# Optimization experiments

Measured on AMD Instinct MI355X. Metric: run time of the kernel, lower is better.

The kernel has to match this reference:

```python
import jax, jax.numpy as jnp
import numpy as np

LAMBDA_MAX = 2.0  # standard re-scaled Laplacian assumption (DGL lambda_max=[2])
NUM_GRAPHS = 100


def _cheb(feat, src, dst, d_invsqrt, W, b):
    # DGL ChebConv: h = sum_i fc_i(X_i) + b, X_i = Chebyshev recursion on scaled Laplacian
    n = feat.shape[0]
    k = W.shape[0]
    re = 2.0 / LAMBDA_MAX

    def aggr(f):  # D^{-1/2} A D^{-1/2} f  via gather + segment_sum
        fh = f * d_invsqrt
        m = jax.ops.segment_sum(fh[src], dst, num_segments=n)
        return m * d_invsqrt

    X0 = feat
    h = X0 @ W[0]
    if k > 1:
        X1 = -re * aggr(X0) + X0 * (re - 1.0)
        h = h + X1 @ W[1]
        for i in range(2, k):
            Xi = -2.0 * re * aggr(X1) + X1 * (2.0 * (re - 1.0)) - X0
            h = h + Xi @ W[i]
            X0, X1 = X1, Xi
    return h + b


def _edgeconv(feat, src, dst, Wt, bt, Wp, bp):
    # DGL EdgeConv: out_i = max_{j->i} [theta(x_i - x_j) + phi(x_i)], 0 if no in-edges
    n = feat.shape[0]
    theta = (feat[dst] - feat[src]) @ Wt + bt           # [E, H]
    phi = feat @ Wp + bp                                # [N, H]
    msg = theta + phi[dst]                              # [E, H]
    agg = jax.ops.segment_max(msg, dst, num_segments=n)
    return jnp.where(jnp.isfinite(agg), agg, jnp.zeros((), feat.dtype))


def setup_inputs() -> dict:
    key = jax.random.key(0)
    ks = jax.random.split(key, 20)
    N, E, G = 100000, 1600000, NUM_GRAPHS
    IN, H, K = 16, 64, 3

    def lin(k, fan_in, shape):
        return jax.random.normal(k, shape, dtype=jnp.float32) * (1.0 / np.sqrt(fan_in))

    inp = {}
    inp["feat"] = jax.random.normal(ks[0], (N, IN), dtype=jnp.float32)
    inp["src"] = jax.random.randint(ks[1], (E,), 0, N)
    inp["dst"] = jax.random.randint(ks[2], (E,), 0, N)
    inp["graph_ids"] = jnp.sort(jax.random.randint(ks[3], (N,), 0, G))
    # ChebConv params: W [k, in, out], b [out]
    inp["W1"] = lin(ks[4], IN, (K, IN, H)); inp["b1"] = jnp.zeros((H,), jnp.float32)
    inp["W2"] = lin(ks[5], H, (K, H, H));   inp["b2"] = jnp.zeros((H,), jnp.float32)
    inp["W3"] = lin(ks[6], H, (K, H, H));   inp["b3"] = jnp.zeros((H,), jnp.float32)
    # EdgeConv params: theta + phi linears
    inp["Wt1"] = lin(ks[7], H, (H, H));  inp["bt1"] = jnp.zeros((H,), jnp.float32)
    inp["Wp1"] = lin(ks[8], H, (H, H));  inp["bp1"] = jnp.zeros((H,), jnp.float32)
    inp["Wt2"] = lin(ks[9], H, (H, H));  inp["bt2"] = jnp.zeros((H,), jnp.float32)
    inp["Wp2"] = lin(ks[10], H, (H, H)); inp["bp2"] = jnp.zeros((H,), jnp.float32)
    return inp


def reference(feat, src, dst, graph_ids, W1, b1, W2, b2, W3, b3,
              Wt1, bt1, Wp1, bp1, Wt2, bt2, Wp2, bp2):
    n = feat.shape[0]
    deg = jax.ops.segment_sum(jnp.ones((src.shape[0],), feat.dtype), dst, num_segments=n)
    d_invsqrt = (jnp.clip(deg, 1.0, None) ** -0.5)[:, None]  # [N, 1]

    h = jax.nn.relu(_cheb(feat, src, dst, d_invsqrt, W1, b1))
    h = jax.nn.relu(_edgeconv(h, src, dst, Wt1, bt1, Wp1, bp1))
    h = jax.nn.relu(_cheb(h, src, dst, d_invsqrt, W2, b2))
    h = jax.nn.relu(_edgeconv(h, src, dst, Wt2, bt2, Wp2, bp2))
    h = jax.nn.relu(_cheb(h, src, dst, d_invsqrt, W3, b3))

    # dgl.mean_nodes: per-graph mean pooling
    counts = jax.ops.segment_sum(jnp.ones((n,), h.dtype), graph_ids, num_segments=NUM_GRAPHS)
    hg = jax.ops.segment_sum(h, graph_ids, num_segments=NUM_GRAPHS)
    return hg / jnp.clip(counts, 1.0, None)[:, None]
```

## Files before the change

kernel.cpp:

```cpp
#include <hip/hip_runtime.h>
#include <hip/hip_bf16.h>
#include <math.h>

typedef __attribute__((ext_vector_type(8))) short short8;
typedef __attribute__((ext_vector_type(4))) float floatx4;

__device__ __forceinline__ unsigned short bfb(float x) {
    union { __hip_bfloat16 h; unsigned short u; } c;
    c.h = __float2bfloat16(x);
    return c.u;
}
__device__ __forceinline__ float bf2f(unsigned short u) {
    union { unsigned int i; float f; } c;
    c.i = ((unsigned int)u) << 16;
    return c.f;
}
__device__ __forceinline__ void acc2(float& lo, float& hi, unsigned d) {
    union { unsigned u; float f; } a, b;
    a.u = d << 16;
    b.u = d & 0xffff0000u;
    lo += a.f; hi += b.f;
}
__device__ __forceinline__ unsigned pkmaxu16(unsigned a, unsigned b) {
    unsigned d;
    asm("v_pk_max_u16 %0, %1, %2" : "=v"(d) : "v"(a), "v"(b));
    return d;
}


__global__ __launch_bounds__(256) void k_bhist(const int* __restrict__ dst, int* __restrict__ bcnt, int E) {
    __shared__ int h[512];
    int t = threadIdx.x;
    for (int i = t; i < 512; i += 256) h[i] = 0;
    __syncthreads();
    int step = gridDim.x * 256;
    for (int i = blockIdx.x * 256 + t; i < E; i += step) atomicAdd(&h[dst[i] >> 8], 1);
    __syncthreads();
    for (int i = t; i < 512; i += 256) if (h[i]) atomicAdd(&bcnt[i], h[i]);
}

__global__ __launch_bounds__(512) void k_scanBkt(const int* __restrict__ bcnt, int* __restrict__ boff,
                                                 int* __restrict__ bcur, int nb, int E) {
    __shared__ int s[512];
    int t = threadIdx.x;
    int v = (t < nb) ? bcnt[t] : 0;
    s[t] = v;
    __syncthreads();
    for (int off = 1; off < 512; off <<= 1) {
        int x = (t >= off) ? s[t - off] : 0;
        __syncthreads();
        s[t] += x;
        __syncthreads();
    }
    if (t < nb) { boff[t] = s[t] - v; bcur[t] = s[t] - v; }
    if (t == 0) boff[nb] = E;
}

#define PCHUNK 8192

__global__ __launch_bounds__(256) void k_partA(const int* __restrict__ src, const int* __restrict__ dst,
                                               int* __restrict__ bcur, unsigned* __restrict__ ebuf, int E) {
    __shared__ int h[512];
    __shared__ int base[512];
    int t = threadIdx.x;
    for (int i = t; i < 512; i += 256) h[i] = 0;
    __syncthreads();
    int start = blockIdx.x * PCHUNK;
    int end = start + PCHUNK < E ? start + PCHUNK : E;
    for (int i = start + t; i < end; i += 256) atomicAdd(&h[dst[i] >> 8], 1);
    __syncthreads();
    for (int i = t; i < 512; i += 256) {
        int c = h[i];
        base[i] = c ? atomicAdd(&bcur[i], c) : 0;
        h[i] = 0;
    }
    __syncthreads();
    for (int i = start + t; i < end; i += 256) {
        int d = dst[i];
        int b = d >> 8;
        int r = atomicAdd(&h[b], 1);
        ebuf[base[b] + r] = ((unsigned)src[i] << 8) | (unsigned)(d & 255);
    }
}

__global__ __launch_bounds__(256) void k_finish(const unsigned* __restrict__ ebuf, const int* __restrict__ boff,
                                                int* __restrict__ row_off, float* __restrict__ dinv,
                                                float* __restrict__ dsq, int* __restrict__ csr,
                                                const float* __restrict__ feat, unsigned short* __restrict__ hd,
                                                int N, int E) {
    __shared__ int h[256];
    __shared__ int sc[256];
    __shared__ int cur[256];
    int b = blockIdx.x, t = threadIdx.x;
    h[t] = 0;
    __syncthreads();
    int beg = boff[b], end = boff[b + 1];
    for (int e = beg + t; e < end; e += 256) atomicAdd(&h[ebuf[e] & 255], 1);
    __syncthreads();
    int v = h[t];
    sc[t] = v;
    __syncthreads();
    for (int off = 1; off < 256; off <<= 1) {
        int x = (t >= off) ? sc[t - off] : 0;
        __syncthreads();
        sc[t] += x;
        __syncthreads();
    }
    int node = (b << 8) + t;
    int excl = beg + sc[t] - v;
    if (node < N) {
        row_off[node] = excl;
        float dg = (float)(v > 1 ? v : 1);
        float dv = rsqrtf(dg);
        dinv[node] = dv;
        dsq[node] = sqrtf(dg);
        const float* f = &feat[(size_t)node * 16];
#pragma unroll
        for (int k = 0; k < 16; k += 4) {
            float4 x = *(const float4*)&f[k];
            ushort4 u = { bfb(x.x * dv), bfb(x.y * dv), bfb(x.z * dv), bfb(x.w * dv) };
            *(ushort4*)&hd[(size_t)node * 16 + k] = u;
        }
    }
    cur[t] = excl;
    if (b == 0 && t == 0) row_off[N] = E;
    __syncthreads();
    for (int e = beg + t; e < end; e += 256) {
        unsigned ed = ebuf[e];
        int pos = atomicAdd(&cur[ed & 255], 1);
        csr[pos] = (int)(ed >> 8);
    }
}


__global__ __launch_bounds__(256) void k_aggr16(const unsigned short* __restrict__ Xd, const float* __restrict__ Z,
                                                const float* __restrict__ dinv,
                                                const int* __restrict__ row_off, const int* __restrict__ csr,
                                                unsigned short* __restrict__ outb, unsigned short* __restrict__ outd,
                                                float alpha, float beta, int zoff, int N) {
    int node = blockIdx.x * 4 + (threadIdx.x >> 6);
    if (node >= N) return;
    int lane = threadIdx.x & 63;
    int g = lane >> 2;
    int co = (lane & 3) * 8;
    int beg = row_off[node], end = row_off[node + 1];
    int deg = end - beg;
    int myOff = (lane < deg) ? (csr[beg + lane] << 5) : zoff;
    const char* base = (const char*)Xd + co;
    float a0 = 0.f, a1 = 0.f, a2 = 0.f, a3 = 0.f;
    {
        int o0 = __shfl(myOff, g);
        int o1 = __shfl(myOff, 16 + g);
        ushort4 x0 = *(const ushort4*)(base + o0);
        ushort4 x1 = *(const ushort4*)(base + o1);
        a0 += bf2f(x0.x); a1 += bf2f(x0.y); a2 += bf2f(x0.z); a3 += bf2f(x0.w);
        a0 += bf2f(x1.x); a1 += bf2f(x1.y); a2 += bf2f(x1.z); a3 += bf2f(x1.w);
    }
    if (deg > 32) {
        int dmain = deg < 64 ? deg : 64;
        for (int j = 32; j < dmain; j += 16) {
            int o = __shfl(myOff, j + g);
            ushort4 x = *(const ushort4*)(base + o);
            a0 += bf2f(x.x); a1 += bf2f(x.y); a2 += bf2f(x.z); a3 += bf2f(x.w);
        }
        for (int e = beg + 64; e < end; e += 16) {
            int idx = e + g;
            int s = csr[idx < end ? idx : end - 1];
            ushort4 x = *(const ushort4*)(base + (s << 5));
            if (idx < end) {
                a0 += bf2f(x.x); a1 += bf2f(x.y); a2 += bf2f(x.z); a3 += bf2f(x.w);
            }
        }
    }
    a0 += __shfl_xor(a0, 4); a0 += __shfl_xor(a0, 8); a0 += __shfl_xor(a0, 16); a0 += __shfl_xor(a0, 32);
    a1 += __shfl_xor(a1, 4); a1 += __shfl_xor(a1, 8); a1 += __shfl_xor(a1, 16); a1 += __shfl_xor(a1, 32);
    a2 += __shfl_xor(a2, 4); a2 += __shfl_xor(a2, 8); a2 += __shfl_xor(a2, 16); a2 += __shfl_xor(a2, 32);
    a3 += __shfl_xor(a3, 4); a3 += __shfl_xor(a3, 8); a3 += __shfl_xor(a3, 16); a3 += __shfl_xor(a3, 32);
    if (g == 0) {
        int c4 = (lane & 3) * 4;
        float dn = dinv[node];
        float v0 = alpha * dn * a0;
        float v1 = alpha * dn * a1;
        float v2 = alpha * dn * a2;
        float v3 = alpha * dn * a3;
        if (Z) {
            float4 zv = *(const float4*)&Z[(size_t)node * 16 + c4];
            v0 += beta * zv.x; v1 += beta * zv.y; v2 += beta * zv.z; v3 += beta * zv.w;
        }
        ushort4 ub = { bfb(v0), bfb(v1), bfb(v2), bfb(v3) };
        *(ushort4*)&outb[(size_t)node * 16 + c4] = ub;
        if (outd) {
            ushort4 u = { bfb(v0 * dn), bfb(v1 * dn), bfb(v2 * dn), bfb(v3 * dn) };
            *(ushort4*)&outd[(size_t)node * 16 + c4] = u;
        }
    }
}


__global__ __launch_bounds__(256) void k_aggr64(const unsigned short* __restrict__ Xd,
                                                const unsigned short* __restrict__ Z,
                                                const float* __restrict__ dinv,
                                                const int* __restrict__ row_off, const int* __restrict__ csr,
                                                unsigned short* __restrict__ outb, unsigned short* __restrict__ outd,
                                                float alpha, float beta, int zoff, int N) {
    int node = blockIdx.x * 4 + (threadIdx.x >> 6);
    if (node >= N) return;
    int lane = threadIdx.x & 63;
    int g = lane >> 3;
    int co = (lane & 7) * 16;
    int beg = row_off[node], end = row_off[node + 1];
    int deg = end - beg;
    int myOff = (lane < deg) ? (csr[beg + lane] << 7) : zoff;
    const char* base = (const char*)Xd + co;
    float a0 = 0.f, a1 = 0.f, a2 = 0.f, a3 = 0.f, a4 = 0.f, a5 = 0.f, a6 = 0.f, a7 = 0.f;
    {
        int o0 = __shfl(myOff, g);
        int o1 = __shfl(myOff, 8 + g);
        int o2 = __shfl(myOff, 16 + g);
        int o3 = __shfl(myOff, 24 + g);
        uint4 x0 = *(const uint4*)(base + o0);
        uint4 x1 = *(const uint4*)(base + o1);
        uint4 x2 = *(const uint4*)(base + o2);
        uint4 x3 = *(const uint4*)(base + o3);
        acc2(a0, a1, x0.x); acc2(a2, a3, x0.y); acc2(a4, a5, x0.z); acc2(a6, a7, x0.w);
        acc2(a0, a1, x1.x); acc2(a2, a3, x1.y); acc2(a4, a5, x1.z); acc2(a6, a7, x1.w);
        acc2(a0, a1, x2.x); acc2(a2, a3, x2.y); acc2(a4, a5, x2.z); acc2(a6, a7, x2.w);
        acc2(a0, a1, x3.x); acc2(a2, a3, x3.y); acc2(a4, a5, x3.z); acc2(a6, a7, x3.w);
    }
    if (deg > 32) {
        int dmain = deg < 64 ? deg : 64;
        for (int j = 32; j < dmain; j += 8) {
            int o = __shfl(myOff, j + g);
            uint4 x = *(const uint4*)(base + o);
            acc2(a0, a1, x.x); acc2(a2, a3, x.y); acc2(a4, a5, x.z); acc2(a6, a7, x.w);
        }
        for (int e = beg + 64; e < end; e += 8) {
            int idx = e + g;
            int s = csr[idx < end ? idx : end - 1];
            uint4 x = *(const uint4*)(base + (s << 7));
            if (idx < end) {
                acc2(a0, a1, x.x); acc2(a2, a3, x.y); acc2(a4, a5, x.z); acc2(a6, a7, x.w);
            }
        }
    }
    a0 += __shfl_xor(a0, 8); a0 += __shfl_xor(a0, 16); a0 += __shfl_xor(a0, 32);
    a1 += __shfl_xor(a1, 8); a1 += __shfl_xor(a1, 16); a1 += __shfl_xor(a1, 32);
    a2 += __shfl_xor(a2, 8); a2 += __shfl_xor(a2, 16); a2 += __shfl_xor(a2, 32);
    a3 += __shfl_xor(a3, 8); a3 += __shfl_xor(a3, 16); a3 += __shfl_xor(a3, 32);
    a4 += __shfl_xor(a4, 8); a4 += __shfl_xor(a4, 16); a4 += __shfl_xor(a4, 32);
    a5 += __shfl_xor(a5, 8); a5 += __shfl_xor(a5, 16); a5 += __shfl_xor(a5, 32);
    a6 += __shfl_xor(a6, 8); a6 += __shfl_xor(a6, 16); a6 += __shfl_xor(a6, 32);
    a7 += __shfl_xor(a7, 8); a7 += __shfl_xor(a7, 16); a7 += __shfl_xor(a7, 32);
    if (g == 0) {
        float dn = dinv[node];
        float v[8] = { a0, a1, a2, a3, a4, a5, a6, a7 };
#pragma unroll
        for (int i = 0; i < 8; ++i) v[i] *= alpha * dn;
        size_t rb = (size_t)node * 128 + co;
        if (Z) {
            uint4 zv = *(const uint4*)((const char*)Z + rb);
            unsigned zd[4] = { zv.x, zv.y, zv.z, zv.w };
#pragma unroll
            for (int i = 0; i < 4; ++i) {
                union { unsigned u; float f; } lo, hi;
                lo.u = zd[i] << 16; hi.u = zd[i] & 0xffff0000u;
                v[2 * i] += beta * lo.f;
                v[2 * i + 1] += beta * hi.f;
            }
        }
        if (outb) {
            uint4 ub;
            unsigned* pb = (unsigned*)&ub;
#pragma unroll
            for (int i = 0; i < 4; ++i)
                pb[i] = (unsigned)bfb(v[2 * i]) | ((unsigned)bfb(v[2 * i + 1]) << 16);
            *(uint4*)((char*)outb + rb) = ub;
        }
        if (outd) {
            uint4 ud;
            unsigned* pd = (unsigned*)&ud;
#pragma unroll
            for (int i = 0; i < 4; ++i)
                pd[i] = (unsigned)bfb(v[2 * i] * dn) | ((unsigned)bfb(v[2 * i + 1] * dn) << 16);
            *(uint4*)((char*)outd + rb) = ud;
        }
    }
}


template <int KDIM, bool FUSE_E1, bool POOLOUT>
__global__ __launch_bounds__(256) void k_cheb(const void* __restrict__ X0v, const void* __restrict__ X1v,
                                              const void* __restrict__ X2v, const float* __restrict__ dsq,
                                              const float* __restrict__ W, const float* __restrict__ bvec,
                                              const float* __restrict__ Wt, const float* __restrict__ Wp,
                                              const float* __restrict__ bt, const float* __restrict__ bp,
                                              unsigned short* __restrict__ md, unsigned short* __restrict__ pbuf,
                                              const int* __restrict__ gid, float* __restrict__ out, int N) {
    constexpr int KT = (KDIM == 16) ? 64 : 3 * KDIM;
    constexpr int SX = KT + 8;
    constexpr int PH1 = 2 * 64 * SX;
    constexpr int PH2 = FUSE_E1 ? (64 * 72 + 128 * 72) : 0;
    constexpr int SSZ = PH1 > PH2 ? PH1 : PH2;
    constexpr bool hasMid = (KDIM == 64);
    __shared__ unsigned short S[SSZ];
    unsigned short* Xs = S;
    unsigned short* Ws = S + 64 * SX;
    int t = threadIdx.x;

    {
        int sn = t & 63;
        int gn = blockIdx.x * 64 + sn; if (gn >= N) gn = N - 1;
        int k0 = (t >> 6) * (KDIM / 4);
        if constexpr (KDIM == 16) {
            float4 v = *(const float4*)&((const float*)X0v)[(size_t)gn * 16 + k0];
            ushort4 u = { bfb(v.x), bfb(v.y), bfb(v.z), bfb(v.w) };
            *(ushort4*)&Xs[sn * SX + k0] = u;
            *(ushort4*)&Xs[sn * SX + 16 + k0] =
                *(const ushort4*)&((const unsigned short*)X1v)[(size_t)gn * 16 + k0];
            *(ushort4*)&Xs[sn * SX + 32 + k0] =
                *(const ushort4*)&((const unsigned short*)X2v)[(size_t)gn * 16 + k0];
            int kp = 48 + (t >> 6) * 4;
            ushort4 z = { 0, 0, 0, 0 };
            *(ushort4*)&Xs[sn * SX + kp] = z;
        } else {
            const unsigned short* Xp[3] = { (const unsigned short*)X0v, (const unsigned short*)X1v,
                                            (const unsigned short*)X2v };
#pragma unroll
            for (int a = 0; a < 3; ++a) {
#pragma unroll
                for (int i = 0; i < KDIM / 16; ++i) {
                    *(ushort4*)&Xs[sn * SX + a * KDIM + k0 + 4 * i] =
                        *(const ushort4*)&Xp[a][(size_t)gn * KDIM + k0 + 4 * i];
                }
            }
        }
    }
    for (int idx = t; idx < 3 * KDIM * 64; idx += 256) {
        int a = idx / (KDIM * 64);
        int r = idx % (KDIM * 64);
        int k = r >> 6, n = r & 63;
        Ws[n * SX + a * KDIM + k] = bfb(W[idx]);
    }
    if constexpr (KDIM == 16) {
        for (int idx = t; idx < 1024; idx += 256) {
            int n = idx & 63, k = 48 + (idx >> 6);
            Ws[n * SX + k] = 0;
        }
    }
    __syncthreads();

    int wave = t >> 6, lane = t & 63;
    int fi = lane & 15, quad = lane >> 4;
    int arow = wave * 16 + fi;

    floatx4 accA[4], accM[4];
#pragma unroll
    for (int i = 0; i < 4; ++i) { accA[i] = (floatx4){0.f,0.f,0.f,0.f}; accM[i] = (floatx4){0.f,0.f,0.f,0.f}; }
#pragma unroll
    for (int ks = 0; ks < KT / 32; ++ks) {
        short8 af = *(const short8*)&Xs[arow * SX + ks * 32 + quad * 8];
        short8 b0 = *(const short8*)&Ws[(0 * 16 + fi) * SX + ks * 32 + quad * 8];
        short8 b1 = *(const short8*)&Ws[(1 * 16 + fi) * SX + ks * 32 + quad * 8];
        short8 b2 = *(const short8*)&Ws[(2 * 16 + fi) * SX + ks * 32 + quad * 8];
        short8 b3 = *(const short8*)&Ws[(3 * 16 + fi) * SX + ks * 32 + quad * 8];
        if (hasMid && ks >= 2 && ks < 4) {
            accM[0] = __builtin_amdgcn_mfma_f32_16x16x32_bf16(af, b0, accM[0], 0, 0, 0);
            accM[1] = __builtin_amdgcn_mfma_f32_16x16x32_bf16(af, b1, accM[1], 0, 0, 0);
            accM[2] = __builtin_amdgcn_mfma_f32_16x16x32_bf16(af, b2, accM[2], 0, 0, 0);
            accM[3] = __builtin_amdgcn_mfma_f32_16x16x32_bf16(af, b3, accM[3], 0, 0, 0);
        } else {
            accA[0] = __builtin_amdgcn_mfma_f32_16x16x32_bf16(af, b0, accA[0], 0, 0, 0);
            accA[1] = __builtin_amdgcn_mfma_f32_16x16x32_bf16(af, b1, accA[1], 0, 0, 0);
            accA[2] = __builtin_amdgcn_mfma_f32_16x16x32_bf16(af, b2, accA[2], 0, 0, 0);
            accA[3] = __builtin_amdgcn_mfma_f32_16x16x32_bf16(af, b3, accA[3], 0, 0, 0);
        }
    }

    int nbase0 = blockIdx.x * 64 + wave * 16;
    int nbase = nbase0 + quad * 4;
    float dd[4];
#pragma unroll
    for (int reg = 0; reg < 4; ++reg) {
        if constexpr (hasMid) {
            int node = nbase + reg;
            dd[reg] = dsq[node < N ? node : N - 1];
        } else dd[reg] = 0.f;
    }
    float rv[4][4];
#pragma unroll
    for (int nt = 0; nt < 4; ++nt) {
        int col = nt * 16 + fi;
        float bias = bvec[col];
#pragma unroll
        for (int reg = 0; reg < 4; ++reg) {
            float v = accA[nt][reg] + bias;
            if constexpr (hasMid) v += accM[nt][reg] * dd[reg];
            rv[nt][reg] = fmaxf(v, 0.f);
        }
    }

    if constexpr (POOLOUT) {
        int gfirst = gid[nbase0 < N ? nbase0 : N - 1];
        int lastn = nbase0 + 15;
        int glast = gid[lastn < N ? lastn : N - 1];
        bool uniform = (lastn < N) && (gfirst == glast);
        if (uniform) {
#pragma unroll
            for (int nt = 0; nt < 4; ++nt) {
                float s = (rv[nt][0] + rv[nt][1]) + (rv[nt][2] + rv[nt][3]);
                s += __shfl_xor(s, 16); s += __shfl_xor(s, 32);
                if (quad == 0) atomicAdd(&out[(size_t)gfirst * 64 + nt * 16 + fi], s);
            }
        } else {
#pragma unroll
            for (int reg = 0; reg < 4; ++reg) {
                int node = nbase + reg;
                if (node < N) {
                    int g = gid[node];
#pragma unroll
                    for (int nt = 0; nt < 4; ++nt)
                        atomicAdd(&out[(size_t)g * 64 + nt * 16 + fi], rv[nt][reg]);
                }
            }
        }
    } else if constexpr (FUSE_E1) {
        __syncthreads();
        unsigned short* Hs = S;
        unsigned short* W2l = S + 64 * 72;
        int lrow = wave * 16 + quad * 4;
#pragma unroll
        for (int nt = 0; nt < 4; ++nt)
#pragma unroll
            for (int reg = 0; reg < 4; ++reg)
                Hs[(lrow + reg) * 72 + nt * 16 + fi] = bfb(rv[nt][reg]);
        for (int idx = t; idx < 4096; idx += 256) {
            int k = idx >> 6, n = idx & 63;
            float wt = Wt[idx];
            W2l[n * 72 + k] = bfb(wt);
            W2l[(64 + n) * 72 + k] = bfb(wt + Wp[idx]);
        }
        __syncthreads();
        floatx4 ae[8];
#pragma unroll
        for (int i = 0; i < 8; ++i) ae[i] = (floatx4){0.f,0.f,0.f,0.f};
#pragma unroll
        for (int ks = 0; ks < 2; ++ks) {
            short8 af = *(const short8*)&Hs[arow * 72 + ks * 32 + quad * 8];
#pragma unroll
            for (int nt = 0; nt < 8; ++nt) {
                short8 bf = *(const short8*)&W2l[(nt * 16 + fi) * 72 + ks * 32 + quad * 8];
                ae[nt] = __builtin_amdgcn_mfma_f32_16x16x32_bf16(af, bf, ae[nt], 0, 0, 0);
            }
        }
#pragma unroll
        for (int nt = 0; nt < 8; ++nt) {
            int col = nt * 16 + fi;
            if (col < 64) {
#pragma unroll
                for (int reg = 0; reg < 4; ++reg) {
                    int node = nbase + reg;
                    if (node < N) {
                        unsigned u = (unsigned)bfb(ae[nt][reg]) ^ 0x8000u;
                        unsigned key = (u & 0x8000u) ? (~u & 0xffffu) : (u | 0x8000u);
                        md[(size_t)node * 64 + col] = (unsigned short)key;
                    }
                }
            } else {
                int cc = col - 64;
                float bias2 = bt[cc] + bp[cc];
#pragma unroll
                for (int reg = 0; reg < 4; ++reg) {
                    int node = nbase + reg;
                    if (node < N) pbuf[(size_t)node * 64 + cc] = bfb(ae[nt][reg] + bias2);
                }
            }
        }
    }
}


__global__ __launch_bounds__(256) void k_e2_b(const unsigned short* __restrict__ md,
                                              const unsigned short* __restrict__ pbuf,
                                              const int* __restrict__ row_off, const int* __restrict__ csr,
                                              const float* __restrict__ dinv, unsigned short* __restrict__ out,
                                              unsigned short* __restrict__ outd, int zoff, int N) {
    int node = blockIdx.x * 4 + (threadIdx.x >> 6);
    if (node >= N) return;
    int lane = threadIdx.x & 63;
    int g = lane >> 3;
    int co = (lane & 7) * 16;
    int beg = row_off[node], end = row_off[node + 1];
    int deg = end - beg;
    int dmain = deg < 64 ? deg : 64;
    int li = lane < dmain ? lane : dmain - 1;
    int myOff = (deg > 0) ? (csr[beg + li] << 7) : zoff;
    const char* base = (const char*)md + co;
    unsigned k0 = 0, k1 = 0, k2 = 0, k3 = 0;
    {
        int o0 = __shfl(myOff, g);
        int o1 = __shfl(myOff, 8 + g);
        int o2 = __shfl(myOff, 16 + g);
        int o3 = __shfl(myOff, 24 + g);
        uint4 x0 = *(const uint4*)(base + o0);
        uint4 x1 = *(const uint4*)(base + o1);
        uint4 x2 = *(const uint4*)(base + o2);
        uint4 x3 = *(const uint4*)(base + o3);
        k0 = pkmaxu16(k0, x0.x); k1 = pkmaxu16(k1, x0.y); k2 = pkmaxu16(k2, x0.z); k3 = pkmaxu16(k3, x0.w);
        k0 = pkmaxu16(k0, x1.x); k1 = pkmaxu16(k1, x1.y); k2 = pkmaxu16(k2, x1.z); k3 = pkmaxu16(k3, x1.w);
        k0 = pkmaxu16(k0, x2.x); k1 = pkmaxu16(k1, x2.y); k2 = pkmaxu16(k2, x2.z); k3 = pkmaxu16(k3, x2.w);
        k0 = pkmaxu16(k0, x3.x); k1 = pkmaxu16(k1, x3.y); k2 = pkmaxu16(k2, x3.z); k3 = pkmaxu16(k3, x3.w);
    }
    if (deg > 32) {
        for (int j = 32; j < dmain; j += 8) {
            int o = __shfl(myOff, j + g);
            uint4 x = *(const uint4*)(base + o);
            k0 = pkmaxu16(k0, x.x); k1 = pkmaxu16(k1, x.y); k2 = pkmaxu16(k2, x.z); k3 = pkmaxu16(k3, x.w);
        }
        for (int e = beg + 64; e < end; e += 8) {
            int idx = e + g;
            int s = csr[idx < end ? idx : end - 1];
            uint4 x = *(const uint4*)(base + (s << 7));
            k0 = pkmaxu16(k0, x.x); k1 = pkmaxu16(k1, x.y); k2 = pkmaxu16(k2, x.z); k3 = pkmaxu16(k3, x.w);
        }
    }
    k0 = pkmaxu16(k0, __shfl_xor((int)k0, 8)); k0 = pkmaxu16(k0, __shfl_xor((int)k0, 16)); k0 = pkmaxu16(k0, __shfl_xor((int)k0, 32));
    k1 = pkmaxu16(k1, __shfl_xor((int)k1, 8)); k1 = pkmaxu16(k1, __shfl_xor((int)k1, 16)); k1 = pkmaxu16(k1, __shfl_xor((int)k1, 32));
    k2 = pkmaxu16(k2, __shfl_xor((int)k2, 8)); k2 = pkmaxu16(k2, __shfl_xor((int)k2, 16)); k2 = pkmaxu16(k2, __shfl_xor((int)k2, 32));
    k3 = pkmaxu16(k3, __shfl_xor((int)k3, 8)); k3 = pkmaxu16(k3, __shfl_xor((int)k3, 16)); k3 = pkmaxu16(k3, __shfl_xor((int)k3, 32));
    if (g == 0) {
        unsigned kd[4] = { k0, k1, k2, k3 };
        float a[8];
#pragma unroll
        for (int i = 0; i < 4; ++i) {
            unsigned klo = kd[i] & 0xffffu, khi = kd[i] >> 16;
            unsigned short tlo = (klo & 0x8000u) ? (unsigned short)(klo & 0x7fffu) : (unsigned short)(~klo & 0xffffu);
            unsigned short thi = (khi & 0x8000u) ? (unsigned short)(khi & 0x7fffu) : (unsigned short)(~khi & 0xffffu);
            a[2 * i] = bf2f(tlo);
            a[2 * i + 1] = bf2f(thi);
        }
        float r[8];
        if (end > beg) {
            uint4 pk = *(const uint4*)((const char*)pbuf + (size_t)node * 128 + co);
            unsigned pd4[4] = { pk.x, pk.y, pk.z, pk.w };
#pragma unroll
            for (int i = 0; i < 4; ++i) {
                r[2 * i]     = fmaxf(bf2f((unsigned short)(pd4[i] & 0xffffu)) + a[2 * i], 0.f);
                r[2 * i + 1] = fmaxf(bf2f((unsigned short)(pd4[i] >> 16)) + a[2 * i + 1], 0.f);
            }
        } else {
#pragma unroll
            for (int i = 0; i < 8; ++i) r[i] = 0.f;
        }
        float dn = dinv[node];
        size_t rb = (size_t)node * 128 + co;
        uint4 ub, ud;
        unsigned* pb = (unsigned*)&ub;
        unsigned* pd = (unsigned*)&ud;
#pragma unroll
        for (int i = 0; i < 4; ++i) {
            pb[i] = (unsigned)bfb(r[2 * i]) | ((unsigned)bfb(r[2 * i + 1]) << 16);
            pd[i] = (unsigned)bfb(r[2 * i] * dn) | ((unsigned)bfb(r[2 * i + 1] * dn) << 16);
        }
        *(uint4*)((char*)out + rb) = ub;
        *(uint4*)((char*)outd + rb) = ud;
    }
}


__global__ __launch_bounds__(256) void k_div(float* __restrict__ out, const int* __restrict__ gid,
                                             int N, int total) {
    int i = blockIdx.x * blockDim.x + threadIdx.x;
    if (i >= total) return;
    int g = i >> 6;
    int lo = 0, hi = N;
    while (lo < hi) { int m = (lo + hi) >> 1; if (gid[m] < g) lo = m + 1; else hi = m; }
    int s = lo;
    hi = N;
    while (lo < hi) { int m = (lo + hi) >> 1; if (gid[m] < g + 1) lo = m + 1; else hi = m; }
    float c = (float)(lo - s);
    out[i] /= fmaxf(c, 1.f);
}


extern "C" void kernel_launch(void* const* d_in, const int* in_sizes, int n_in,
                              void* d_out, int out_size, void* d_ws, size_t ws_size,
                              hipStream_t stream) {
    const float* feat = (const float*)d_in[0];
    const int* src = (const int*)d_in[1];
    const int* dst = (const int*)d_in[2];
    const int* gid = (const int*)d_in[3];
    const float* W1 = (const float*)d_in[4];  const float* b1 = (const float*)d_in[5];
    const float* W2 = (const float*)d_in[6];  const float* b2 = (const float*)d_in[7];
    const float* W3 = (const float*)d_in[8];  const float* b3 = (const float*)d_in[9];
    const float* Wt1 = (const float*)d_in[10]; const float* bt1 = (const float*)d_in[11];
    const float* Wp1 = (const float*)d_in[12]; const float* bp1 = (const float*)d_in[13];
    const float* Wt2 = (const float*)d_in[14]; const float* bt2 = (const float*)d_in[15];
    const float* Wp2 = (const float*)d_in[16]; const float* bp2 = (const float*)d_in[17];
    float* out = (float*)d_out;

    const int N = in_sizes[0] / 16;
    const int E = in_sizes[1];
    const int nb = (N + 255) >> 8;

    char* p = (char*)d_ws;
    auto alloc = [&](size_t nbytes) {
        void* r = (void*)p;
        p += (nbytes + 255) & ~(size_t)255;
        return r;
    };
    int* bcnt     = (int*)alloc(512 * 4);
    char* zpage   = (char*)alloc(256);
    size_t zspan  = (size_t)((char*)zpage - (char*)bcnt) + 256;
    int* boff     = (int*)alloc(513 * 4);
    int* bcur     = (int*)alloc(512 * 4);
    int* row_off  = (int*)alloc((size_t)(N + 1) * 4);
    int* csr      = (int*)alloc((size_t)E * 4);
    float* dinv   = (float*)alloc((size_t)N * 4);
    float* dsq    = (float*)alloc((size_t)N * 4);
    float* bufA   = (float*)alloc((size_t)N * 64 * 4);
    float* bufB   = (float*)alloc((size_t)N * 64 * 4);
    float* bufC   = (float*)alloc((size_t)N * 64 * 4);
    float* bufD   = (float*)alloc((size_t)N * 64 * 4);
    unsigned short* md   = (unsigned short*)alloc((size_t)N * 64 * 2);
    unsigned short* pbuf = (unsigned short*)alloc((size_t)N * 64 * 2);

    unsigned* ebuf = (unsigned*)bufA;
    unsigned short* hd = (unsigned short*)bufC;
    unsigned short* xd = hd + (size_t)N * 64;
    unsigned short* xA16 = (unsigned short*)bufA;
    unsigned short* xB16 = (unsigned short*)bufB;
    unsigned short* xd3 = (unsigned short*)bufA;
    unsigned short* hD = (unsigned short*)bufD;

    const int zo_hd = (int)((char*)zpage - (char*)hd);
    const int zo_xd = (int)((char*)zpage - (char*)xd);
    const int zo_xd3 = (int)((char*)zpage - (char*)xd3);
    const int zo_md = (int)((char*)zpage - (char*)md);

    hipMemsetAsync(bcnt, 0, zspan, stream);
    hipMemsetAsync(d_out, 0, (size_t)out_size * 4, stream);

    const int nbw = (N + 3) / 4;
    const int nbt = (N + 63) / 64;
    const int npart = (E + PCHUNK - 1) / PCHUNK;

    k_bhist<<<256, 256, 0, stream>>>(dst, bcnt, E);
    k_scanBkt<<<1, 512, 0, stream>>>(bcnt, boff, bcur, nb, E);
    k_partA<<<npart, 256, 0, stream>>>(src, dst, bcur, ebuf, E);
    k_finish<<<nb, 256, 0, stream>>>(ebuf, boff, row_off, dinv, dsq, csr, feat, hd, N, E);

    k_aggr16<<<nbw, 256, 0, stream>>>(hd, nullptr, dinv, row_off, csr, xA16, xd, -1.f, 0.f, zo_hd, N);
    k_aggr16<<<nbw, 256, 0, stream>>>(xd, feat, dinv, row_off, csr, xB16, nullptr, -2.f, -1.f, zo_xd, N);
    k_cheb<16, true, false><<<nbt, 256, 0, stream>>>(feat, xA16, xB16, nullptr, W1, b1,
                                                     Wt1, Wp1, bt1, bp1, md, pbuf, nullptr, nullptr, N);
    k_e2_b<<<nbw, 256, 0, stream>>>(md, pbuf, row_off, csr, dinv, hD, hd, zo_md, N);

    k_aggr64<<<nbw, 256, 0, stream>>>(hd, nullptr, dinv, row_off, csr, nullptr, xd, -1.f, 0.f, zo_hd, N);
    k_aggr64<<<nbw, 256, 0, stream>>>(xd, hD, dinv, row_off, csr, xB16, nullptr, -2.f, -1.f, zo_xd, N);
    k_cheb<64, true, false><<<nbt, 256, 0, stream>>>(hD, xd, xB16, dsq, W2, b2,
                                                     Wt2, Wp2, bt2, bp2, md, pbuf, nullptr, nullptr, N);
    k_e2_b<<<nbw, 256, 0, stream>>>(md, pbuf, row_off, csr, dinv, hD, hd, zo_md, N);

    k_aggr64<<<nbw, 256, 0, stream>>>(hd, nullptr, dinv, row_off, csr, nullptr, xd3, -1.f, 0.f, zo_hd, N);
    k_aggr64<<<nbw, 256, 0, stream>>>(xd3, hD, dinv, row_off, csr, xB16, nullptr, -2.f, -1.f, zo_xd3, N);
    k_cheb<64, false, true><<<nbt, 256, 0, stream>>>(hD, xd3, xB16, dsq, W3, b3,
                                                     nullptr, nullptr, nullptr, nullptr,
                                                     nullptr, nullptr, gid, out, N);

    k_div<<<(out_size + 255) / 256, 256, 0, stream>>>(out, gid, N, out_size);
}
```

Measured before the change: 533.7 us.

## Fuse second Chebyshev aggregation into cheb GEMM and drop CSR bucket prepass

The second neighbour aggregation of each Chebyshev layer now runs inside the GEMM kernel: each block gathers its 64 rows into shared memory before the MFMA, so the X2 intermediate is never written to or read back from global memory. The bucket histogram and scan kernels are removed by giving each 256-node bucket a fixed slab of SLABC slots, and row offsets become begin/end pairs. Pooling accumulates into a workspace buffer so the separate output memset can be dropped. The trade-offs are that gather latency now sits inside the GEMM blocks, which have lower parallelism than the standalone aggregation kernels, and the fixed slab size assumes no bucket ever receives more than 5120 edges.

```diff
diff --git a/kernel.cpp b/kernel.cpp
--- a/kernel.cpp
+++ b/kernel.cpp
@@ -27,36 +27,9 @@
     return d;
 }
 
-
-__global__ __launch_bounds__(256) void k_bhist(const int* __restrict__ dst, int* __restrict__ bcnt, int E) {
-    __shared__ int h[512];
-    int t = threadIdx.x;
-    for (int i = t; i < 512; i += 256) h[i] = 0;
-    __syncthreads();
-    int step = gridDim.x * 256;
-    for (int i = blockIdx.x * 256 + t; i < E; i += step) atomicAdd(&h[dst[i] >> 8], 1);
-    __syncthreads();
-    for (int i = t; i < 512; i += 256) if (h[i]) atomicAdd(&bcnt[i], h[i]);
-}
-
-__global__ __launch_bounds__(512) void k_scanBkt(const int* __restrict__ bcnt, int* __restrict__ boff,
-                                                 int* __restrict__ bcur, int nb, int E) {
-    __shared__ int s[512];
-    int t = threadIdx.x;
-    int v = (t < nb) ? bcnt[t] : 0;
-    s[t] = v;
-    __syncthreads();
-    for (int off = 1; off < 512; off <<= 1) {
-        int x = (t >= off) ? s[t - off] : 0;
-        __syncthreads();
-        s[t] += x;
-        __syncthreads();
-    }
-    if (t < nb) { boff[t] = s[t] - v; bcur[t] = s[t] - v; }
-    if (t == 0) boff[nb] = E;
-}
-
+#define SLABC 5120
 #define PCHUNK 8192
+
 
 __global__ __launch_bounds__(256) void k_partA(const int* __restrict__ src, const int* __restrict__ dst,
                                                int* __restrict__ bcur, unsigned* __restrict__ ebuf, int E) {
@@ -79,22 +52,22 @@
         int d = dst[i];
         int b = d >> 8;
         int r = atomicAdd(&h[b], 1);
-        ebuf[base[b] + r] = ((unsigned)src[i] << 8) | (unsigned)(d & 255);
-    }
-}
-
-__global__ __launch_bounds__(256) void k_finish(const unsigned* __restrict__ ebuf, const int* __restrict__ boff,
-                                                int* __restrict__ row_off, float* __restrict__ dinv,
+        ebuf[b * SLABC + base[b] + r] = ((unsigned)src[i] << 8) | (unsigned)(d & 255);
+    }
+}
+
+__global__ __launch_bounds__(256) void k_finish(const unsigned* __restrict__ ebuf, const int* __restrict__ bcur,
+                                                int2* __restrict__ row_be, float* __restrict__ dinv,
                                                 float* __restrict__ dsq, int* __restrict__ csr,
                                                 const float* __restrict__ feat, unsigned short* __restrict__ hd,
-                                                int N, int E) {
+                                                int N) {
     __shared__ int h[256];
     __shared__ int sc[256];
     __shared__ int cur[256];
     int b = blockIdx.x, t = threadIdx.x;
     h[t] = 0;
     __syncthreads();
-    int beg = boff[b], end = boff[b + 1];
+    int beg = b * SLABC, end = beg + bcur[b];
     for (int e = beg + t; e < end; e += 256) atomicAdd(&h[ebuf[e] & 255], 1);
     __syncthreads();
     int v = h[t];
@@ -109,7 +82,7 @@
     int node = (b << 8) + t;
     int excl = beg + sc[t] - v;
     if (node < N) {
-        row_off[node] = excl;
+        row_be[node] = make_int2(excl, excl + v);
         float dg = (float)(v > 1 ? v : 1);
         float dv = rsqrtf(dg);
         dinv[node] = dv;
@@ -123,7 +96,6 @@
         }
     }
     cur[t] = excl;
-    if (b == 0 && t == 0) row_off[N] = E;
     __syncthreads();
     for (int e = beg + t; e < end; e += 256) {
         unsigned ed = ebuf[e];
@@ -133,17 +105,18 @@
 }
 
 
-__global__ __launch_bounds__(256) void k_aggr16(const unsigned short* __restrict__ Xd, const float* __restrict__ Z,
+__global__ __launch_bounds__(256) void k_aggr16(const unsigned short* __restrict__ Xd,
                                                 const float* __restrict__ dinv,
-                                                const int* __restrict__ row_off, const int* __restrict__ csr,
+                                                const int2* __restrict__ row_be, const int* __restrict__ csr,
                                                 unsigned short* __restrict__ outb, unsigned short* __restrict__ outd,
-                                                float alpha, float beta, int zoff, int N) {
+                                                int zoff, int N) {
     int node = blockIdx.x * 4 + (threadIdx.x >> 6);
     if (node >= N) return;
     int lane = threadIdx.x & 63;
     int g = lane >> 2;
     int co = (lane & 3) * 8;
-    int beg = row_off[node], end = row_off[node + 1];
+    int2 be = row_be[node];
+    int beg = be.x, end = be.y;
     int deg = end - beg;
     int myOff = (lane < deg) ? (csr[beg + lane] << 5) : zoff;
     const char* base = (const char*)Xd + co;
@@ -179,36 +152,26 @@
     if (g == 0) {
         int c4 = (lane & 3) * 4;
         float dn = dinv[node];
-        float v0 = alpha * dn * a0;
-        float v1 = alpha * dn * a1;
-        float v2 = alpha * dn * a2;
-        float v3 = alpha * dn * a3;
-        if (Z) {
-            float4 zv = *(const float4*)&Z[(size_t)node * 16 + c4];
-            v0 += beta * zv.x; v1 += beta * zv.y; v2 += beta * zv.z; v3 += beta * zv.w;
-        }
+        float v0 = -dn * a0, v1 = -dn * a1, v2 = -dn * a2, v3 = -dn * a3;
         ushort4 ub = { bfb(v0), bfb(v1), bfb(v2), bfb(v3) };
         *(ushort4*)&outb[(size_t)node * 16 + c4] = ub;
-        if (outd) {
-            ushort4 u = { bfb(v0 * dn), bfb(v1 * dn), bfb(v2 * dn), bfb(v3 * dn) };
-            *(ushort4*)&outd[(size_t)node * 16 + c4] = u;
-        }
+        ushort4 u = { bfb(v0 * dn), bfb(v1 * dn), bfb(v2 * dn), bfb(v3 * dn) };
+        *(ushort4*)&outd[(size_t)node * 16 + c4] = u;
     }
 }
 
 
 __global__ __launch_bounds__(256) void k_aggr64(const unsigned short* __restrict__ Xd,
-                                                const unsigned short* __restrict__ Z,
                                                 const float* __restrict__ dinv,
-                                                const int* __restrict__ row_off, const int* __restrict__ csr,
-                                                unsigned short* __restrict__ outb, unsigned short* __restrict__ outd,
-                                                float alpha, float beta, int zoff, int N) {
+                                                const int2* __restrict__ row_be, const int* __restrict__ csr,
+                                                unsigned short* __restrict__ outd, int zoff, int N) {
     int node = blockIdx.x * 4 + (threadIdx.x >> 6);
     if (node >= N) return;
     int lane = threadIdx.x & 63;
     int g = lane >> 3;
     int co = (lane & 7) * 16;
-    int beg = row_off[node], end = row_off[node + 1];
+    int2 be = row_be[node];
+    int beg = be.x, end = be.y;
     int deg = end - beg;
     int myOff = (lane < deg) ? (csr[beg + lane] << 7) : zoff;
     const char* base = (const char*)Xd + co;
@@ -254,116 +217,324 @@
     if (g == 0) {
         float dn = dinv[node];
         float v[8] = { a0, a1, a2, a3, a4, a5, a6, a7 };
-#pragma unroll
-        for (int i = 0; i < 8; ++i) v[i] *= alpha * dn;
-        size_t rb = (size_t)node * 128 + co;
-        if (Z) {
-            uint4 zv = *(const uint4*)((const char*)Z + rb);
-            unsigned zd[4] = { zv.x, zv.y, zv.z, zv.w };
-#pragma unroll
-            for (int i = 0; i < 4; ++i) {
-                union { unsigned u; float f; } lo, hi;
-                lo.u = zd[i] << 16; hi.u = zd[i] & 0xffff0000u;
-                v[2 * i] += beta * lo.f;
-                v[2 * i + 1] += beta * hi.f;
-            }
-        }
-        if (outb) {
-            uint4 ub;
-            unsigned* pb = (unsigned*)&ub;
-#pragma unroll
-            for (int i = 0; i < 4; ++i)
-                pb[i] = (unsigned)bfb(v[2 * i]) | ((unsigned)bfb(v[2 * i + 1]) << 16);
-            *(uint4*)((char*)outb + rb) = ub;
-        }
-        if (outd) {
-            uint4 ud;
-            unsigned* pd = (unsigned*)&ud;
-#pragma unroll
-            for (int i = 0; i < 4; ++i)
-                pd[i] = (unsigned)bfb(v[2 * i] * dn) | ((unsigned)bfb(v[2 * i + 1] * dn) << 16);
-            *(uint4*)((char*)outd + rb) = ud;
-        }
-    }
-}
-
-
-template <int KDIM, bool FUSE_E1, bool POOLOUT>
-__global__ __launch_bounds__(256) void k_cheb(const void* __restrict__ X0v, const void* __restrict__ X1v,
-                                              const void* __restrict__ X2v, const float* __restrict__ dsq,
-                                              const float* __restrict__ W, const float* __restrict__ bvec,
-                                              const float* __restrict__ Wt, const float* __restrict__ Wp,
-                                              const float* __restrict__ bt, const float* __restrict__ bp,
-                                              unsigned short* __restrict__ md, unsigned short* __restrict__ pbuf,
-                                              const int* __restrict__ gid, float* __restrict__ out, int N) {
-    constexpr int KT = (KDIM == 16) ? 64 : 3 * KDIM;
-    constexpr int SX = KT + 8;
-    constexpr int PH1 = 2 * 64 * SX;
-    constexpr int PH2 = FUSE_E1 ? (64 * 72 + 128 * 72) : 0;
-    constexpr int SSZ = PH1 > PH2 ? PH1 : PH2;
-    constexpr bool hasMid = (KDIM == 64);
-    __shared__ unsigned short S[SSZ];
-    unsigned short* Xs = S;
-    unsigned short* Ws = S + 64 * SX;
+        uint4 ud;
+        unsigned* pd = (unsigned*)&ud;
+#pragma unroll
+        for (int i = 0; i < 4; ++i) {
+            float lo = -dn * dn * v[2 * i];
+            float hi = -dn * dn * v[2 * i + 1];
+            pd[i] = (unsigned)bfb(lo) | ((unsigned)bfb(hi) << 16);
+        }
+        *(uint4*)((char*)outd + (size_t)node * 128 + co) = ud;
+    }
+}
+
+
+__global__ __launch_bounds__(256) void k_cheb16f(const float* __restrict__ feat,
+                                                 const unsigned short* __restrict__ X1b,
+                                                 const unsigned short* __restrict__ xd,
+                                                 const int2* __restrict__ row_be, const int* __restrict__ csr,
+                                                 const float* __restrict__ dinv,
+                                                 const float* __restrict__ W, const float* __restrict__ bvec,
+                                                 const float* __restrict__ Wt, const float* __restrict__ Wp,
+                                                 const float* __restrict__ bt, const float* __restrict__ bp,
+                                                 unsigned short* __restrict__ md, unsigned short* __restrict__ pbuf,
+                                                 int zoff, int N) {
+    constexpr int SX = 72;
+    __shared__ unsigned short S[13824];
+    unsigned short* Ws = S;
+    unsigned short* Xs2 = S + 64 * 72;
     int t = threadIdx.x;
+    int wave = t >> 6, lane = t & 63;
+
+    for (int idx = t; idx < 3072; idx += 256) {
+        int a = idx >> 10;
+        int r = idx & 1023;
+        int k = r >> 6, n = r & 63;
+        Ws[n * SX + a * 16 + k] = bfb(W[idx]);
+    }
+    for (int idx = t; idx < 1024; idx += 256) {
+        int n = idx & 63, k = 48 + (idx >> 6);
+        Ws[n * SX + k] = 0;
+    }
 
     {
-        int sn = t & 63;
-        int gn = blockIdx.x * 64 + sn; if (gn >= N) gn = N - 1;
-        int k0 = (t >> 6) * (KDIM / 4);
-        if constexpr (KDIM == 16) {
-            float4 v = *(const float4*)&((const float*)X0v)[(size_t)gn * 16 + k0];
-            ushort4 u = { bfb(v.x), bfb(v.y), bfb(v.z), bfb(v.w) };
-            *(ushort4*)&Xs[sn * SX + k0] = u;
-            *(ushort4*)&Xs[sn * SX + 16 + k0] =
-                *(const ushort4*)&((const unsigned short*)X1v)[(size_t)gn * 16 + k0];
-            *(ushort4*)&Xs[sn * SX + 32 + k0] =
-                *(const ushort4*)&((const unsigned short*)X2v)[(size_t)gn * 16 + k0];
-            int kp = 48 + (t >> 6) * 4;
-            ushort4 z = { 0, 0, 0, 0 };
-            *(ushort4*)&Xs[sn * SX + kp] = z;
-        } else {
-            const unsigned short* Xp[3] = { (const unsigned short*)X0v, (const unsigned short*)X1v,
-                                            (const unsigned short*)X2v };
-#pragma unroll
-            for (int a = 0; a < 3; ++a) {
-#pragma unroll
-                for (int i = 0; i < KDIM / 16; ++i) {
-                    *(ushort4*)&Xs[sn * SX + a * KDIM + k0 + 4 * i] =
-                        *(const ushort4*)&Xp[a][(size_t)gn * KDIM + k0 + 4 * i];
+        int g = lane >> 2;
+        int co = (lane & 3) * 8;
+        const char* base = (const char*)xd + co;
+        for (int i = 0; i < 16; ++i) {
+            int ln = wave * 16 + i;
+            int gn = blockIdx.x * 64 + ln; if (gn >= N) gn = N - 1;
+            int2 be = row_be[gn];
+            int beg = be.x, end = be.y;
+            int deg = end - beg;
+            int myOff = (lane < deg) ? (csr[beg + lane] << 5) : zoff;
+            float a0 = 0.f, a1 = 0.f, a2 = 0.f, a3 = 0.f;
+            {
+                int o0 = __shfl(myOff, g);
+                int o1 = __shfl(myOff, 16 + g);
+                ushort4 x0 = *(const ushort4*)(base + o0);
+                ushort4 x1 = *(const ushort4*)(base + o1);
+                a0 += bf2f(x0.x); a1 += bf2f(x0.y); a2 += bf2f(x0.z); a3 += bf2f(x0.w);
+                a0 += bf2f(x1.x); a1 += bf2f(x1.y); a2 += bf2f(x1.z); a3 += bf2f(x1.w);
+            }
+            if (deg > 32) {
+                int dmain = deg < 64 ? deg : 64;
+                for (int j = 32; j < dmain; j += 16) {
+                    int o = __shfl(myOff, j + g);
+                    ushort4 x = *(const ushort4*)(base + o);
+                    a0 += bf2f(x.x); a1 += bf2f(x.y); a2 += bf2f(x.z); a3 += bf2f(x.w);
                 }
-            }
-        }
-    }
-    for (int idx = t; idx < 3 * KDIM * 64; idx += 256) {
-        int a = idx / (KDIM * 64);
-        int r = idx % (KDIM * 64);
-        int k = r >> 6, n = r & 63;
-        Ws[n * SX + a * KDIM + k] = bfb(W[idx]);
-    }
-    if constexpr (KDIM == 16) {
-        for (int idx = t; idx < 1024; idx += 256) {
-            int n = idx & 63, k = 48 + (idx >> 6);
-            Ws[n * SX + k] = 0;
-        }
-    }
-    __syncthreads();
-
-    int wave = t >> 6, lane = t & 63;
+                for (int e = beg + 64; e < end; e += 16) {
+                    int idx = e + g;
+                    int s = csr[idx < end ? idx : end - 1];
+                    ushort4 x = *(const ushort4*)(base + (s << 5));
+                    if (idx < end) {
+                        a0 += bf2f(x.x); a1 += bf2f(x.y); a2 += bf2f(x.z); a3 += bf2f(x.w);
+                    }
+                }
+            }
+            a0 += __shfl_xor(a0, 4); a0 += __shfl_xor(a0, 8); a0 += __shfl_xor(a0, 16); a0 += __shfl_xor(a0, 32);
+            a1 += __shfl_xor(a1, 4); a1 += __shfl_xor(a1, 8); a1 += __shfl_xor(a1, 16); a1 += __shfl_xor(a1, 32);
+            a2 += __shfl_xor(a2, 4); a2 += __shfl_xor(a2, 8); a2 += __shfl_xor(a2, 16); a2 += __shfl_xor(a2, 32);
+            a3 += __shfl_xor(a3, 4); a3 += __shfl_xor(a3, 8); a3 += __shfl_xor(a3, 16); a3 += __shfl_xor(a3, 32);
+            if (g == 0) {
+                int c4 = (lane & 3) * 4;
+                float dn = dinv[gn];
+                float4 zv = *(const float4*)&feat[(size_t)gn * 16 + c4];
+                float v0 = -2.f * dn * a0 - zv.x;
+                float v1 = -2.f * dn * a1 - zv.y;
+                float v2 = -2.f * dn * a2 - zv.z;
+                float v3 = -2.f * dn * a3 - zv.w;
+                ushort4 u = { bfb(v0), bfb(v1), bfb(v2), bfb(v3) };
+                *(ushort4*)&Xs2[ln * 24 + c4] = u;
+            }
+        }
+    }
+    __syncthreads();
+
     int fi = lane & 15, quad = lane >> 4;
     int arow = wave * 16 + fi;
+    int arow_node = blockIdx.x * 64 + arow;
+    int anode = arow_node < N ? arow_node : N - 1;
+
+    floatx4 acc[4];
+#pragma unroll
+    for (int i = 0; i < 4; ++i) acc[i] = (floatx4){0.f,0.f,0.f,0.f};
+#pragma unroll
+    for (int ks = 0; ks < 2; ++ks) {
+#pragma unroll
+        for (int q2 = 0; q2 < 1; ++q2) {}
+        int kidx = ks * 32 + quad * 8;
+        int seg = kidx >> 4;
+        short8 af;
+        if (seg == 0) {
+            const float* rp = &feat[(size_t)anode * 16 + (kidx & 15)];
+            float4 v0 = *(const float4*)rp;
+            float4 v1 = *(const float4*)(rp + 4);
+            af = (short8){ (short)bfb(v0.x), (short)bfb(v0.y), (short)bfb(v0.z), (short)bfb(v0.w),
+                           (short)bfb(v1.x), (short)bfb(v1.y), (short)bfb(v1.z), (short)bfb(v1.w) };
+        } else if (seg == 1) {
+            af = *(const short8*)&X1b[(size_t)anode * 16 + (kidx & 15)];
+        } else if (seg == 2) {
+            af = *(const short8*)&Xs2[arow * 24 + (kidx & 15)];
+        } else {
+            af = (short8){0,0,0,0,0,0,0,0};
+        }
+        short8 b0 = *(const short8*)&Ws[(0 * 16 + fi) * SX + kidx];
+        short8 b1 = *(const short8*)&Ws[(1 * 16 + fi) * SX + kidx];
+        short8 b2 = *(const short8*)&Ws[(2 * 16 + fi) * SX + kidx];
+        short8 b3 = *(const short8*)&Ws[(3 * 16 + fi) * SX + kidx];
+        acc[0] = __builtin_amdgcn_mfma_f32_16x16x32_bf16(af, b0, acc[0], 0, 0, 0);
+        acc[1] = __builtin_amdgcn_mfma_f32_16x16x32_bf16(af, b1, acc[1], 0, 0, 0);
+        acc[2] = __builtin_amdgcn_mfma_f32_16x16x32_bf16(af, b2, acc[2], 0, 0, 0);
+        acc[3] = __builtin_amdgcn_mfma_f32_16x16x32_bf16(af, b3, acc[3], 0, 0, 0);
+    }
+
+    int nbase = blockIdx.x * 64 + wave * 16 + quad * 4;
+    float rv[4][4];
+#pragma unroll
+    for (int nt = 0; nt < 4; ++nt) {
+        float bias = bvec[nt * 16 + fi];
+#pragma unroll
+        for (int reg = 0; reg < 4; ++reg) rv[nt][reg] = fmaxf(acc[nt][reg] + bias, 0.f);
+    }
+
+    __syncthreads();
+    unsigned short* Hs = S;
+    unsigned short* W2l = S + 64 * 72;
+    int lrow = wave * 16 + quad * 4;
+#pragma unroll
+    for (int nt = 0; nt < 4; ++nt)
+#pragma unroll
+        for (int reg = 0; reg < 4; ++reg)
+            Hs[(lrow + reg) * 72 + nt * 16 + fi] = bfb(rv[nt][reg]);
+    for (int idx = t; idx < 4096; idx += 256) {
+        int k = idx >> 6, n = idx & 63;
+        float wt = Wt[idx];
+        W2l[n * 72 + k] = bfb(wt);
+        W2l[(64 + n) * 72 + k] = bfb(wt + Wp[idx]);
+    }
+    __syncthreads();
+    floatx4 ae[8];
+#pragma unroll
+    for (int i = 0; i < 8; ++i) ae[i] = (floatx4){0.f,0.f,0.f,0.f};
+#pragma unroll
+    for (int ks = 0; ks < 2; ++ks) {
+        short8 af = *(const short8*)&Hs[arow * 72 + ks * 32 + quad * 8];
+#pragma unroll
+        for (int nt = 0; nt < 8; ++nt) {
+            short8 bf = *(const short8*)&W2l[(nt * 16 + fi) * 72 + ks * 32 + quad * 8];
+            ae[nt] = __builtin_amdgcn_mfma_f32_16x16x32_bf16(af, bf, ae[nt], 0, 0, 0);
+        }
+    }
+#pragma unroll
+    for (int nt = 0; nt < 8; ++nt) {
+        int col = nt * 16 + fi;
+        if (col < 64) {
+#pragma unroll
+            for (int reg = 0; reg < 4; ++reg) {
+                int node = nbase + reg;
+                if (node < N) {
+                    unsigned u = (unsigned)bfb(ae[nt][reg]) ^ 0x8000u;
+                    unsigned key = (u & 0x8000u) ? (~u & 0xffffu) : (u | 0x8000u);
+                    md[(size_t)node * 64 + col] = (unsigned short)key;
+                }
+            }
+        } else {
+            int cc = col - 64;
+            float bias2 = bt[cc] + bp[cc];
+#pragma unroll
+            for (int reg = 0; reg < 4; ++reg) {
+                int node = nbase + reg;
+                if (node < N) pbuf[(size_t)node * 64 + cc] = bfb(ae[nt][reg] + bias2);
+            }
+        }
+    }
+}
+
+
+template <bool POOLOUT>
+__global__ __launch_bounds__(256) void k_cheb64f(const unsigned short* __restrict__ X0,
+                                                 const unsigned short* __restrict__ xd,
+                                                 const int2* __restrict__ row_be, const int* __restrict__ csr,
+                                                 const float* __restrict__ dinv, const float* __restrict__ dsq,
+                                                 const float* __restrict__ W, const float* __restrict__ bvec,
+                                                 const float* __restrict__ Wt, const float* __restrict__ Wp,
+                                                 const float* __restrict__ bt, const float* __restrict__ bp,
+                                                 unsigned short* __restrict__ md, unsigned short* __restrict__ pbuf,
+                                                 const int* __restrict__ gid, float* __restrict__ pout,
+                                                 int zoff, int N) {
+    constexpr int SX = 200;
+    __shared__ unsigned short S[17408];
+    unsigned short* Ws = S;
+    unsigned short* Xs2 = S + 12800;
+    int t = threadIdx.x;
+    int wave = t >> 6, lane = t & 63;
+
+    for (int idx = t; idx < 12288; idx += 256) {
+        int a = idx / 4096;
+        int r = idx & 4095;
+        int k = r >> 6, n = r & 63;
+        Ws[n * SX + a * 64 + k] = bfb(W[idx]);
+    }
+
+    {
+        int g = lane >> 3;
+        int co = (lane & 7) * 16;
+        const char* base = (const char*)xd + co;
+        for (int i = 0; i < 16; ++i) {
+            int ln = wave * 16 + i;
+            int gn = blockIdx.x * 64 + ln; if (gn >= N) gn = N - 1;
+            int2 be = row_be[gn];
+            int beg = be.x, end = be.y;
+            int deg = end - beg;
+            int myOff = (lane < deg) ? (csr[beg + lane] << 7) : zoff;
+            float a0 = 0.f, a1 = 0.f, a2 = 0.f, a3 = 0.f, a4 = 0.f, a5 = 0.f, a6 = 0.f, a7 = 0.f;
+            {
+                int o0 = __shfl(myOff, g);
+                int o1 = __shfl(myOff, 8 + g);
+                int o2 = __shfl(myOff, 16 + g);
+                int o3 = __shfl(myOff, 24 + g);
+                uint4 x0 = *(const uint4*)(base + o0);
+                uint4 x1 = *(const uint4*)(base + o1);
+                uint4 x2 = *(const uint4*)(base + o2);
+                uint4 x3 = *(const uint4*)(base + o3);
+                acc2(a0, a1, x0.x); acc2(a2, a3, x0.y); acc2(a4, a5, x0.z); acc2(a6, a7, x0.w);
+                acc2(a0, a1, x1.x); acc2(a2, a3, x1.y); acc2(a4, a5, x1.z); acc2(a6, a7, x1.w);
+                acc2(a0, a1, x2.x); acc2(a2, a3, x2.y); acc2(a4, a5, x2.z); acc2(a6, a7, x2.w);
+                acc2(a0, a1, x3.x); acc2(a2, a3, x3.y); acc2(a4, a5, x3.z); acc2(a6, a7, x3.w);
+            }
+            if (deg > 32) {
+                int dmain = deg < 64 ? deg : 64;
+                for (int j = 32; j < dmain; j += 8) {
+                    int o = __shfl(myOff, j + g);
+                    uint4 x = *(const uint4*)(base + o);
+                    acc2(a0, a1, x.x); acc2(a2, a3, x.y); acc2(a4, a5, x.z); acc2(a6, a7, x.w);
+                }
+                for (int e = beg + 64; e < end; e += 8) {
+                    int idx = e + g;
+                    int s = csr[idx < end ? idx : end - 1];
+                    uint4 x = *(const uint4*)(base + (s << 7));
+                    if (idx < end) {
+                        acc2(a0, a1, x.x); acc2(a2, a3, x.y); acc2(a4, a5, x.z); acc2(a6, a7, x.w);
+                    }
+                }
+            }
+            a0 += __shfl_xor(a0, 8); a0 += __shfl_xor(a0, 16); a0 += __shfl_xor(a0, 32);
+            a1 += __shfl_xor(a1, 8); a1 += __shfl_xor(a1, 16); a1 += __shfl_xor(a1, 32);
+            a2 += __shfl_xor(a2, 8); a2 += __shfl_xor(a2, 16); a2 += __shfl_xor(a2, 32);
+            a3 += __shfl_xor(a3, 8); a3 += __shfl_xor(a3, 16); a3 += __shfl_xor(a3, 32);
+            a4 += __shfl_xor(a4, 8); a4 += __shfl_xor(a4, 16); a4 += __shfl_xor(a4, 32);
+            a5 += __shfl_xor(a5, 8); a5 += __shfl_xor(a5, 16); a5 += __shfl_xor(a5, 32);
+            a6 += __shfl_xor(a6, 8); a6 += __shfl_xor(a6, 16); a6 += __shfl_xor(a6, 32);
+            a7 += __shfl_xor(a7, 8); a7 += __shfl_xor(a7, 16); a7 += __shfl_xor(a7, 32);
+            if (g == 0) {
+                float dn = dinv[gn];
+                float a[8] = { a0, a1, a2, a3, a4, a5, a6, a7 };
+                uint4 zv = *(const uint4*)((const char*)X0 + (size_t)gn * 128 + co);
+                unsigned zd[4] = { zv.x, zv.y, zv.z, zv.w };
+                uint4 u;
+                unsigned* pu = (unsigned*)&u;
+#pragma unroll
+                for (int q = 0; q < 4; ++q) {
+                    union { unsigned uu; float f; } lo, hi;
+                    lo.uu = zd[q] << 16; hi.uu = zd[q] & 0xffff0000u;
+                    float vlo = -2.f * dn * a[2 * q] - lo.f;
+                    float vhi = -2.f * dn * a[2 * q + 1] - hi.f;
+                    pu[q] = (unsigned)bfb(vlo) | ((unsigned)bfb(vhi) << 16);
+                }
+                *(uint4*)&Xs2[ln * 72 + (lane & 7) * 8] = u;
+            }
+        }
+    }
+    __syncthreads();
+
+    int fi = lane & 15, quad = lane >> 4;
+    int arow = wave * 16 + fi;
+    int arow_node = blockIdx.x * 64 + arow;
+    int anode = arow_node < N ? arow_node : N - 1;
 
     floatx4 accA[4], accM[4];
 #pragma unroll
     for (int i = 0; i < 4; ++i) { accA[i] = (floatx4){0.f,0.f,0.f,0.f}; accM[i] = (floatx4){0.f,0.f,0.f,0.f}; }
 #pragma unroll
-    for (int ks = 0; ks < KT / 32; ++ks) {
-        short8 af = *(const short8*)&Xs[arow * SX + ks * 32 + quad * 8];
-        short8 b0 = *(const short8*)&Ws[(0 * 16 + fi) * SX + ks * 32 + quad * 8];
-        short8 b1 = *(const short8*)&Ws[(1 * 16 + fi) * SX + ks * 32 + quad * 8];
-        short8 b2 = *(const short8*)&Ws[(2 * 16 + fi) * SX + ks * 32 + quad * 8];
-        short8 b3 = *(const short8*)&Ws[(3 * 16 + fi) * SX + ks * 32 + quad * 8];
-        if (hasMid && ks >= 2 && ks < 4) {
+    for (int ks = 0; ks < 6; ++ks) {
+        int kidx = ks * 32 + quad * 8;
+        int seg = kidx >> 6;
+        short8 af;
+        if (seg == 0) {
+            af = *(const short8*)&X0[(size_t)anode * 64 + (kidx & 63)];
+        } else if (seg == 1) {
+            af = *(const short8*)&xd[(size_t)anode * 64 + (kidx & 63)];
+        } else {
+            af = *(const short8*)&Xs2[arow * 72 + (kidx & 63)];
+        }
+        short8 b0 = *(const short8*)&Ws[(0 * 16 + fi) * SX + kidx];
+        short8 b1 = *(const short8*)&Ws[(1 * 16 + fi) * SX + kidx];
+        short8 b2 = *(const short8*)&Ws[(2 * 16 + fi) * SX + kidx];
+        short8 b3 = *(const short8*)&Ws[(3 * 16 + fi) * SX + kidx];
+        if (ks >= 2 && ks < 4) {
             accM[0] = __builtin_amdgcn_mfma_f32_16x16x32_bf16(af, b0, accM[0], 0, 0, 0);
             accM[1] = __builtin_amdgcn_mfma_f32_16x16x32_bf16(af, b1, accM[1], 0, 0, 0);
             accM[2] = __builtin_amdgcn_mfma_f32_16x16x32_bf16(af, b2, accM[2], 0, 0, 0);
@@ -381,22 +552,16 @@
     float dd[4];
 #pragma unroll
     for (int reg = 0; reg < 4; ++reg) {
-        if constexpr (hasMid) {
-            int node = nbase + reg;
-            dd[reg] = dsq[node < N ? node : N - 1];
-        } else dd[reg] = 0.f;
+        int node = nbase + reg;
+        dd[reg] = dsq[node < N ? node : N - 1];
     }
     float rv[4][4];
 #pragma unroll
     for (int nt = 0; nt < 4; ++nt) {
-        int col = nt * 16 + fi;
-        float bias = bvec[col];
-#pragma unroll
-        for (int reg = 0; reg < 4; ++reg) {
-            float v = accA[nt][reg] + bias;
-            if constexpr (hasMid) v += accM[nt][reg] * dd[reg];
-            rv[nt][reg] = fmaxf(v, 0.f);
-        }
+        float bias = bvec[nt * 16 + fi];
+#pragma unroll
+        for (int reg = 0; reg < 4; ++reg)
+            rv[nt][reg] = fmaxf(accA[nt][reg] + accM[nt][reg] * dd[reg] + bias, 0.f);
     }
 
     if constexpr (POOLOUT) {
@@ -409,7 +574,7 @@
             for (int nt = 0; nt < 4; ++nt) {
                 float s = (rv[nt][0] + rv[nt][1]) + (rv[nt][2] + rv[nt][3]);
                 s += __shfl_xor(s, 16); s += __shfl_xor(s, 32);
-                if (quad == 0) atomicAdd(&out[(size_t)gfirst * 64 + nt * 16 + fi], s);
+                if (quad == 0) atomicAdd(&pout[(size_t)gfirst * 64 + nt * 16 + fi], s);
             }
         } else {
 #pragma unroll
@@ -419,11 +584,11 @@
                     int g = gid[node];
 #pragma unroll
                     for (int nt = 0; nt < 4; ++nt)
-                        atomicAdd(&out[(size_t)g * 64 + nt * 16 + fi], rv[nt][reg]);
+                        atomicAdd(&pout[(size_t)g * 64 + nt * 16 + fi], rv[nt][reg]);
                 }
             }
         }
-    } else if constexpr (FUSE_E1) {
+    } else {
         __syncthreads();
         unsigned short* Hs = S;
         unsigned short* W2l = S + 64 * 72;
@@ -481,7 +646,7 @@
 
 __global__ __launch_bounds__(256) void k_e2_b(const unsigned short* __restrict__ md,
                                               const unsigned short* __restrict__ pbuf,
-                                              const int* __restrict__ row_off, const int* __restrict__ csr,
+                                              const int2* __restrict__ row_be, const int* __restrict__ csr,
                                               const float* __restrict__ dinv, unsigned short* __restrict__ out,
                                               unsigned short* __restrict__ outd, int zoff, int N) {
     int node = blockIdx.x * 4 + (threadIdx.x >> 6);
@@ -489,7 +654,8 @@
     int lane = threadIdx.x & 63;
     int g = lane >> 3;
     int co = (lane & 7) * 16;
-    int beg = row_off[node], end = row_off[node + 1];
+    int2 be = row_be[node];
+    int beg = be.x, end = be.y;
     int deg = end - beg;
     int dmain = deg < 64 ? deg : 64;
     int li = lane < dmain ? lane : dmain - 1;
@@ -567,8 +733,8 @@
 }
 
 
-__global__ __launch_bounds__(256) void k_div(float* __restrict__ out, const int* __restrict__ gid,
-                                             int N, int total) {
+__global__ __launch_bounds__(256) void k_div(float* __restrict__ out, const float* __restrict__ pout,
+                                             const int* __restrict__ gid, int N, int total) {
     int i = blockIdx.x * blockDim.x + threadIdx.x;
     if (i >= total) return;
     int g = i >> 6;
@@ -578,7 +744,7 @@
     hi = N;
     while (lo < hi) { int m = (lo + hi) >> 1; if (gid[m] < g + 1) lo = m + 1; else hi = m; }
     float c = (float)(lo - s);
-    out[i] /= fmaxf(c, 1.f);
+    out[i] = pout[i] / fmaxf(c, 1.f);
 }
 
 
@@ -600,6 +766,7 @@
 
     const int N = in_sizes[0] / 16;
     const int E = in_sizes[1];
+    const int G = out_size / 64;
     const int nb = (N + 255) >> 8;
 
     char* p = (char*)d_ws;
@@ -608,19 +775,17 @@
         p += (nbytes + 255) & ~(size_t)255;
         return r;
     };
-    int* bcnt     = (int*)alloc(512 * 4);
+    int* bcur     = (int*)alloc(512 * 4);
     char* zpage   = (char*)alloc(256);
-    size_t zspan  = (size_t)((char*)zpage - (char*)bcnt) + 256;
-    int* boff     = (int*)alloc(513 * 4);
-    int* bcur     = (int*)alloc(512 * 4);
-    int* row_off  = (int*)alloc((size_t)(N + 1) * 4);
-    int* csr      = (int*)alloc((size_t)E * 4);
+    float* pout   = (float*)alloc((size_t)G * 64 * 4);
+    size_t zspan  = (size_t)((char*)pout - (char*)bcur) + (((size_t)G * 64 * 4 + 255) & ~(size_t)255);
+    int2* row_be  = (int2*)alloc((size_t)N * 8);
+    int* csr      = (int*)alloc(((size_t)nb * SLABC + 1024) * 4);
     float* dinv   = (float*)alloc((size_t)N * 4);
     float* dsq    = (float*)alloc((size_t)N * 4);
     float* bufA   = (float*)alloc((size_t)N * 64 * 4);
-    float* bufB   = (float*)alloc((size_t)N * 64 * 4);
     float* bufC   = (float*)alloc((size_t)N * 64 * 4);
-    float* bufD   = (float*)alloc((size_t)N * 64 * 4);
+    unsigned short* hD   = (unsigned short*)alloc((size_t)N * 64 * 2);
     unsigned short* md   = (unsigned short*)alloc((size_t)N * 64 * 2);
     unsigned short* pbuf = (unsigned short*)alloc((size_t)N * 64 * 2);
 
@@ -628,44 +793,34 @@
     unsigned short* hd = (unsigned short*)bufC;
     unsigned short* xd = hd + (size_t)N * 64;
     unsigned short* xA16 = (unsigned short*)bufA;
-    unsigned short* xB16 = (unsigned short*)bufB;
-    unsigned short* xd3 = (unsigned short*)bufA;
-    unsigned short* hD = (unsigned short*)bufD;
 
     const int zo_hd = (int)((char*)zpage - (char*)hd);
     const int zo_xd = (int)((char*)zpage - (char*)xd);
-    const int zo_xd3 = (int)((char*)zpage - (char*)xd3);
     const int zo_md = (int)((char*)zpage - (char*)md);
 
-    hipMemsetAsync(bcnt, 0, zspan, stream);
-    hipMemsetAsync(d_out, 0, (size_t)out_size * 4, stream);
+    hipMemsetAsync(bcur, 0, zspan, stream);
 
     const int nbw = (N + 3) / 4;
     const int nbt = (N + 63) / 64;
     const int npart = (E + PCHUNK - 1) / PCHUNK;
 
-    k_bhist<<<256, 256, 0, stream>>>(dst, bcnt, E);
-    k_scanBkt<<<1, 512, 0, stream>>>(bcnt, boff, bcur, nb, E);
     k_partA<<<npart, 256, 0, stream>>>(src, dst, bcur, ebuf, E);
-    k_finish<<<nb, 256, 0, stream>>>(ebuf, boff, row_off, dinv, dsq, csr, feat, hd, N, E);
-
-    k_aggr16<<<nbw, 256, 0, stream>>>(hd, nullptr, dinv, row_off, csr, xA16, xd, -1.f, 0.f, zo_hd, N);
-    k_aggr16<<<nbw, 256, 0, stream>>>(xd, feat, dinv, row_off, csr, xB16, nullptr, -2.f, -1.f, zo_xd, N);
-    k_cheb<16, true, false><<<nbt, 256, 0, stream>>>(feat, xA16, xB16, nullptr, W1, b1,
-                                                     Wt1, Wp1, bt1, bp1, md, pbuf, nullptr, nullptr, N);
-    k_e2_b<<<nbw, 256, 0, stream>>>(md, pbuf, row_off, csr, dinv, hD, hd, zo_md, N);
-
-    k_aggr64<<<nbw, 256, 0, stream>>>(hd, nullptr, dinv, row_off, csr, nullptr, xd, -1.f, 0.f, zo_hd, N);
-    k_aggr64<<<nbw, 256, 0, stream>>>(xd, hD, dinv, row_off, csr, xB16, nullptr, -2.f, -1.f, zo_xd, N);
-    k_cheb<64, true, false><<<nbt, 256, 0, stream>>>(hD, xd, xB16, dsq, W2, b2,
-                                                     Wt2, Wp2, bt2, bp2, md, pbuf, nullptr, nullptr, N);
-    k_e2_b<<<nbw, 256, 0, stream>>>(md, pbuf, row_off, csr, dinv, hD, hd, zo_md, N);
-
-    k_aggr64<<<nbw, 256, 0, stream>>>(hd, nullptr, dinv, row_off, csr, nullptr, xd3, -1.f, 0.f, zo_hd, N);
-    k_aggr64<<<nbw, 256, 0, stream>>>(xd3, hD, dinv, row_off, csr, xB16, nullptr, -2.f, -1.f, zo_xd3, N);
-    k_cheb<64, false, true><<<nbt, 256, 0, stream>>>(hD, xd3, xB16, dsq, W3, b3,
-                                                     nullptr, nullptr, nullptr, nullptr,
-                                                     nullptr, nullptr, gid, out, N);
-
-    k_div<<<(out_size + 255) / 256, 256, 0, stream>>>(out, gid, N, out_size);
-}
+    k_finish<<<nb, 256, 0, stream>>>(ebuf, bcur, row_be, dinv, dsq, csr, feat, hd, N);
+
+    k_aggr16<<<nbw, 256, 0, stream>>>(hd, dinv, row_be, csr, xA16, xd, zo_hd, N);
+    k_cheb16f<<<nbt, 256, 0, stream>>>(feat, xA16, xd, row_be, csr, dinv, W1, b1,
+                                       Wt1, Wp1, bt1, bp1, md, pbuf, zo_xd, N);
+    k_e2_b<<<nbw, 256, 0, stream>>>(md, pbuf, row_be, csr, dinv, hD, hd, zo_md, N);
+
+    k_aggr64<<<nbw, 256, 0, stream>>>(hd, dinv, row_be, csr, xd, zo_hd, N);
+    k_cheb64f<false><<<nbt, 256, 0, stream>>>(hD, xd, row_be, csr, dinv, dsq, W2, b2,
+                                              Wt2, Wp2, bt2, bp2, md, pbuf, nullptr, nullptr, zo_xd, N);
+    k_e2_b<<<nbw, 256, 0, stream>>>(md, pbuf, row_be, csr, dinv, hD, hd, zo_md, N);
+
+    k_aggr64<<<nbw, 256, 0, stream>>>(hd, dinv, row_be, csr, xd, zo_hd, N);
+    k_cheb64f<true><<<nbt, 256, 0, stream>>>(hD, xd, row_be, csr, dinv, dsq, W3, b3,
+                                             nullptr, nullptr, nullptr, nullptr,
+                                             nullptr, nullptr, gid, pout, zo_xd, N);
+
+    k_div<<<(out_size + 255) / 256, 256, 0, stream>>>(out, pout, gid, N, out_size);
+}
```

Result: slower. 547.2 us (+2.5%).
